# Kernel optimization log

Hardware: AMD Instinct MI355X
Metric: run time of the kernel (lower is better)

## Reference

```python
import jax, jax.numpy as jnp
import numpy as np

N = 50000
E = 800000
D = 128
L = 3


def gru_cell(m, h, w_ih, w_hh, b_ih, b_hh):
    # m, h: [N, D]; w_ih, w_hh: [3D, D]; b_ih, b_hh: [3D]
    gi = m @ w_ih.T + b_ih  # [N, 3D]
    gh = h @ w_hh.T + b_hh  # [N, 3D]
    i_r, i_z, i_n = jnp.split(gi, 3, axis=-1)
    h_r, h_z, h_n = jnp.split(gh, 3, axis=-1)
    r = jax.nn.sigmoid(i_r + h_r)
    z = jax.nn.sigmoid(i_z + h_z)
    n = jnp.tanh(i_n + r * h_n)
    return (1.0 - z) * n + z * h


def setup_inputs() -> dict:
    key = jax.random.key(0)
    ks = jax.random.split(key, 8)
    s = 1.0 / np.sqrt(D)
    z = jax.random.normal(ks[0], (N, D), dtype=jnp.float32)
    edge_index = jax.random.randint(ks[1], (2, E), 0, N, dtype=jnp.int64)
    weight = jax.random.uniform(ks[2], (L, D, D), dtype=jnp.float32, minval=-s, maxval=s)
    w_ih = jax.random.uniform(ks[3], (3 * D, D), dtype=jnp.float32, minval=-s, maxval=s)
    w_hh = jax.random.uniform(ks[4], (3 * D, D), dtype=jnp.float32, minval=-s, maxval=s)
    b_ih = jax.random.uniform(ks[5], (3 * D,), dtype=jnp.float32, minval=-s, maxval=s)
    b_hh = jax.random.uniform(ks[6], (3 * D,), dtype=jnp.float32, minval=-s, maxval=s)
    return {"z": z, "edge_index": edge_index, "weight": weight,
            "w_ih": w_ih, "w_hh": w_hh, "b_ih": b_ih, "b_hh": b_hh}


def reference(z, edge_index, weight, w_ih, w_hh, b_ih, b_hh):
    # GatedGraphConv: per layer, m = h @ W_l; aggregate m[src] into dst (sum); GRU update.
    src, dst = edge_index[0], edge_index[1]
    h = z  # in_channels == out_channels, no padding
    for l in range(L):
        m = h @ weight[l]                              # [N, D]
        agg = jax.ops.segment_sum(m[src], dst, num_segments=N)  # scatter-add over edges
        h = gru_cell(agg, h, w_ih, w_hh, b_ih, b_hh)
    return h
```

## Files before the change

kernel.cpp:

```cpp
#include <hip/hip_runtime.h>
#include <hip/hip_bf16.h>

#define NN 50000
#define NE 800000
#define D 128
#define NL 3
#define G3 384

typedef __attribute__((ext_vector_type(4))) float f32x4;
typedef __attribute__((ext_vector_type(2))) float f32x2;
typedef _Float16 f16;
typedef __attribute__((ext_vector_type(8))) _Float16 f16x8;
typedef __attribute__((ext_vector_type(2))) _Float16 f16x2;

__global__ void detect_i64_kernel(const int* __restrict__ ei, int* __restrict__ flag) {
    __shared__ int any_nz;
    if (threadIdx.x == 0) any_nz = 0;
    __syncthreads();
    int v = ei[threadIdx.x * 2 + 1];
    if (v != 0) atomicOr(&any_nz, 1);
    __syncthreads();
    if (threadIdx.x == 0) *flag = (any_nz == 0) ? 1 : 0;
}

static __device__ __forceinline__ void load_edge(const int* ei, const int* flag, int e,
                                                 int& src, int& dst) {
    if (*flag) {
        src = ei[2LL * e];
        dst = ei[2LL * (NE + e)];
    } else {
        src = ei[e];
        dst = ei[NE + e];
    }
}

__global__ void hist_kernel(const int* __restrict__ ei, const int* __restrict__ flag,
                            int* __restrict__ counts, unsigned short* __restrict__ rank16) {
    int e = blockIdx.x * blockDim.x + threadIdx.x;
    if (e >= NE) return;
    int src, dst;
    load_edge(ei, flag, e, src, dst);
    rank16[e] = (unsigned short)atomicAdd(counts + dst, 1);
}

#define SBLK 256
#define NSB ((NN + SBLK - 1) / SBLK)

__global__ __launch_bounds__(SBLK) void scan_reduce_kernel(const int* __restrict__ counts,
                                                           int* __restrict__ block_sums) {
    __shared__ int lds[SBLK];
    int i = blockIdx.x * SBLK + threadIdx.x;
    lds[threadIdx.x] = (i < NN) ? counts[i] : 0;
    __syncthreads();
    for (int off = SBLK / 2; off > 0; off >>= 1) {
        if (threadIdx.x < off) lds[threadIdx.x] += lds[threadIdx.x + off];
        __syncthreads();
    }
    if (threadIdx.x == 0) block_sums[blockIdx.x] = lds[0];
}

__global__ __launch_bounds__(256) void scan_offsets_kernel(const int* __restrict__ block_sums,
                                                           int* __restrict__ block_off,
                                                           int* __restrict__ row_start) {
    __shared__ int lds[256];
    int t = threadIdx.x;
    int v = (t < NSB) ? block_sums[t] : 0;
    lds[t] = v;
    __syncthreads();
    for (int off = 1; off < 256; off <<= 1) {
        int x = (t >= off) ? lds[t - off] : 0;
        __syncthreads();
        lds[t] += x;
        __syncthreads();
    }
    if (t < NSB) block_off[t] = lds[t] - v;
    if (t == 255) row_start[NN] = lds[255];
}

__global__ __launch_bounds__(SBLK) void scan_final_kernel(const int* __restrict__ counts,
                                                          const int* __restrict__ block_off,
                                                          int* __restrict__ row_start) {
    __shared__ int lds[SBLK];
    int i = blockIdx.x * SBLK + threadIdx.x;
    int v = (i < NN) ? counts[i] : 0;
    lds[threadIdx.x] = v;
    __syncthreads();
    for (int off = 1; off < SBLK; off <<= 1) {
        int x = (threadIdx.x >= off) ? lds[threadIdx.x - off] : 0;
        __syncthreads();
        lds[threadIdx.x] += x;
        __syncthreads();
    }
    if (i < NN) row_start[i] = block_off[blockIdx.x] + lds[threadIdx.x] - v;
}

__global__ void fill_kernel(const int* __restrict__ ei, const int* __restrict__ flag,
                            const int* __restrict__ row_start,
                            const unsigned short* __restrict__ rank16,
                            unsigned short* __restrict__ csr16) {
    int e = blockIdx.x * blockDim.x + threadIdx.x;
    if (e >= NE) return;
    int src, dst;
    load_edge(ei, flag, e, src, dst);
    csr16[row_start[dst] + (int)rank16[e]] = (unsigned short)src;
}

__global__ void init_h_kernel(const float* __restrict__ z, f16* __restrict__ h) {
    int i = blockIdx.x * blockDim.x + threadIdx.x;
    if (i * 2 >= NN * D) return;
    f32x2 v = *(const f32x2*)(z + i * 2);
    f16x2 o = {(f16)v[0], (f16)v[1]};
    *(f16x2*)(h + i * 2) = o;
}

__global__ __launch_bounds__(256) void gather_kernel(
    const f16* __restrict__ h, const int* __restrict__ row_start,
    const unsigned short* __restrict__ csr16, f16* __restrict__ agg) {
    int row = blockIdx.x * 4 + (threadIdx.x >> 6);
    if (row >= NN) return;
    int lane = threadIdx.x & 63;
    int eslot = lane >> 4;
    int c0 = (lane & 15) * 8;
    int beg = row_start[row], end = row_start[row + 1];
    float acc[8] = {0.f, 0.f, 0.f, 0.f, 0.f, 0.f, 0.f, 0.f};
    float acc2[8] = {0.f, 0.f, 0.f, 0.f, 0.f, 0.f, 0.f, 0.f};
    int e = beg;
    for (; e + 7 < end; e += 8) {
        int s0 = (int)csr16[e + eslot];
        int s1 = (int)csr16[e + eslot + 4];
        f16x8 v0 = *(const f16x8*)(h + s0 * D + c0);
        f16x8 v1 = *(const f16x8*)(h + s1 * D + c0);
#pragma unroll
        for (int j = 0; j < 8; ++j) { acc[j] += (float)v0[j]; acc2[j] += (float)v1[j]; }
    }
    for (; e + eslot < end; e += 4) {
        int s = (int)csr16[e + eslot];
        f16x8 v = *(const f16x8*)(h + s * D + c0);
#pragma unroll
        for (int j = 0; j < 8; ++j) acc[j] += (float)v[j];
    }
#pragma unroll
    for (int j = 0; j < 8; ++j) {
        acc[j] += acc2[j];
        acc[j] += __shfl_xor(acc[j], 16, 64);
        acc[j] += __shfl_xor(acc[j], 32, 64);
    }
    if (lane < 16) {
        f16x8 o;
#pragma unroll
        for (int j = 0; j < 8; ++j) o[j] = (f16)acc[j];
        *(f16x8*)(agg + row * D + c0) = o;
    }
}

__global__ void precompute_weights(const float* __restrict__ weight,
                                   const float* __restrict__ w_ih,
                                   const float* __restrict__ w_hh,
                                   f16* __restrict__ wct, f16* __restrict__ whh) {
    int l = blockIdx.x / G3;
    int g = blockIdx.x % G3;
    int c = threadIdx.x;
    __shared__ float wih_row[D];
    wih_row[c] = w_ih[g * D + c];
    __syncthreads();
    const float* wrow = weight + ((long long)l * D + c) * D;
    float acc = 0.f;
#pragma unroll 8
    for (int j = 0; j < D; ++j) acc += wrow[j] * wih_row[j];
    wct[((long long)l * G3 + g) * D + c] = (f16)acc;
    if (l == 0) whh[g * D + c] = (f16)w_hh[g * D + c];
}

#define TMG 128
#define NDT 2
#define MFMA_F16 __builtin_amdgcn_mfma_f32_16x16x32_f16
__global__ __launch_bounds__(512) void gru_fused_kernel(
    const f16* __restrict__ agg, const f16* __restrict__ hin, f16* __restrict__ hout,
    const f16* __restrict__ wct, const f16* __restrict__ whh,
    const float* __restrict__ b_ih, const float* __restrict__ b_hh,
    float* __restrict__ out_f32) {
    __shared__ char wlds[NDT * 6 * 4096];
    const int tid = threadIdx.x;
    const int lane = tid & 63;
    const int wv = tid >> 6;
    const int fr = lane & 15;
    const int kg = lane >> 4;
    const int m0 = blockIdx.x * TMG;
    const int dt0 = blockIdx.y * NDT;

    int arow = m0 + wv * 16 + fr;
    int arc = arow < NN ? arow : NN - 1;
    const int abase = arc * D;

    f16x8 fa[4], fh[4];
#pragma unroll
    for (int ks = 0; ks < 4; ++ks) {
        int k0 = ks * 32 + kg * 8;
        fa[ks] = *(const f16x8*)(agg + abase + k0);
        fh[ks] = *(const f16x8*)(hin + abase + k0);
    }

#pragma unroll
    for (int p6 = 0; p6 < NDT * 3; ++p6) {
        int unit = tid + p6 * 512;
        int dpanel = unit >> 8;
        int dti = dpanel / 6;
        int panel = dpanel % 6;
        int u = unit & 255;
        int sr = u >> 4;
        int sc = (u & 15) * 8;
        int gr = (dt0 + dti) * 16;
        const f16* srcp = (panel < 3)
                              ? wct + (panel * 128 + gr + sr) * D + sc
                              : whh + ((panel - 3) * 128 + gr + sr) * D + sc;
        int wb = (u * 16) ^ ((sr & 7) << 4);
        *(f16x8*)(wlds + dpanel * 4096 + wb) = *(const f16x8*)srcp;
    }
    __syncthreads();

#pragma unroll
    for (int dti = 0; dti < NDT; ++dti) {
        const int gr = (dt0 + dti) * 16;
        const char* wb0 = wlds + dti * 6 * 4096;
        f32x4 a_ir = {0, 0, 0, 0}, a_iz = {0, 0, 0, 0}, a_in = {0, 0, 0, 0};
        f32x4 a_hr = {0, 0, 0, 0}, a_hz = {0, 0, 0, 0}, a_hn = {0, 0, 0, 0};
#pragma unroll
        for (int ks = 0; ks < 4; ++ks) {
            const int kb = fr * 256 + (((ks * 4 + kg) ^ (fr & 7)) << 4);
            f16x8 bir = *(const f16x8*)(wb0 + 0 * 4096 + kb);
            f16x8 biz = *(const f16x8*)(wb0 + 1 * 4096 + kb);
            f16x8 bin = *(const f16x8*)(wb0 + 2 * 4096 + kb);
            f16x8 bhr = *(const f16x8*)(wb0 + 3 * 4096 + kb);
            f16x8 bhz = *(const f16x8*)(wb0 + 4 * 4096 + kb);
            f16x8 bhn = *(const f16x8*)(wb0 + 5 * 4096 + kb);
            a_ir = MFMA_F16(fa[ks], bir, a_ir, 0, 0, 0);
            a_iz = MFMA_F16(fa[ks], biz, a_iz, 0, 0, 0);
            a_in = MFMA_F16(fa[ks], bin, a_in, 0, 0, 0);
            a_hr = MFMA_F16(fh[ks], bhr, a_hr, 0, 0, 0);
            a_hz = MFMA_F16(fh[ks], bhz, a_hz, 0, 0, 0);
            a_hn = MFMA_F16(fh[ks], bhn, a_hn, 0, 0, 0);
        }
        const int d = gr + fr;
        float bir_ = b_ih[d], biz_ = b_ih[128 + d], bin_ = b_ih[256 + d];
        float bhr_ = b_hh[d], bhz_ = b_hh[128 + d], bhn_ = b_hh[256 + d];
#pragma unroll
        for (int j = 0; j < 4; ++j) {
            int row = m0 + wv * 16 + kg * 4 + j;
            if (row >= NN) continue;
            float ir = a_ir[j] + bir_, iz = a_iz[j] + biz_, in_ = a_in[j] + bin_;
            float hr = a_hr[j] + bhr_, hz = a_hz[j] + bhz_, hn = a_hn[j] + bhn_;
            float r = 1.f / (1.f + __expf(-(ir + hr)));
            float zz = 1.f / (1.f + __expf(-(iz + hz)));
            float e2 = __expf(2.f * (in_ + r * hn));
            float nn = 1.f - 2.f / (e2 + 1.f);
            int off = row * D + d;
            float hold = (float)hin[off];
            float hnew = (1.f - zz) * nn + zz * hold;
            if (out_f32)
                out_f32[off] = hnew;
            else
                hout[off] = (f16)hnew;
        }
    }
}

__global__ __launch_bounds__(256) void gru_fused_fallback(
    const f16* __restrict__ agg, const f16* __restrict__ hin, f16* __restrict__ hout,
    const f16* __restrict__ wct, const f16* __restrict__ whh,
    const float* __restrict__ b_ih, const float* __restrict__ b_hh,
    float* __restrict__ out_f32) {
    const int tid = threadIdx.x;
    const int lane = tid & 63;
    const int wv = tid >> 6;
    const int fr = lane & 15;
    const int kg = lane >> 4;
    const int m0 = blockIdx.x * 64;
    int arow = m0 + wv * 16 + fr;
    int arc = arow < NN ? arow : NN - 1;
    const int abase = arc * D;
    f16x8 fa[4], fh[4];
#pragma unroll
    for (int ks = 0; ks < 4; ++ks) {
        int k0 = ks * 32 + kg * 8;
        fa[ks] = *(const f16x8*)(agg + abase + k0);
        fh[ks] = *(const f16x8*)(hin + abase + k0);
    }
#pragma unroll 1
    for (int dt = 0; dt < 8; ++dt) {
        const int g = dt * 16 + fr;
        f32x4 a_ir = {0, 0, 0, 0}, a_iz = {0, 0, 0, 0}, a_in = {0, 0, 0, 0};
        f32x4 a_hr = {0, 0, 0, 0}, a_hz = {0, 0, 0, 0}, a_hn = {0, 0, 0, 0};
#pragma unroll
        for (int ks = 0; ks < 4; ++ks) {
            int k0 = ks * 32 + kg * 8;
            f16x8 bir = *(const f16x8*)(wct + (g)*D + k0);
            f16x8 biz = *(const f16x8*)(wct + (128 + g) * D + k0);
            f16x8 bin = *(const f16x8*)(wct + (256 + g) * D + k0);
            f16x8 bhr = *(const f16x8*)(whh + (g)*D + k0);
            f16x8 bhz = *(const f16x8*)(whh + (128 + g) * D + k0);
            f16x8 bhn = *(const f16x8*)(whh + (256 + g) * D + k0);
            a_ir = MFMA_F16(fa[ks], bir, a_ir, 0, 0, 0);
            a_iz = MFMA_F16(fa[ks], biz, a_iz, 0, 0, 0);
            a_in = MFMA_F16(fa[ks], bin, a_in, 0, 0, 0);
            a_hr = MFMA_F16(fh[ks], bhr, a_hr, 0, 0, 0);
            a_hz = MFMA_F16(fh[ks], bhz, a_hz, 0, 0, 0);
            a_hn = MFMA_F16(fh[ks], bhn, a_hn, 0, 0, 0);
        }
        const int d = g;
        float bir_ = b_ih[d], biz_ = b_ih[128 + d], bin_ = b_ih[256 + d];
        float bhr_ = b_hh[d], bhz_ = b_hh[128 + d], bhn_ = b_hh[256 + d];
#pragma unroll
        for (int j = 0; j < 4; ++j) {
            int row = m0 + wv * 16 + kg * 4 + j;
            if (row >= NN) continue;
            float ir = a_ir[j] + bir_, iz = a_iz[j] + biz_, in_ = a_in[j] + bin_;
            float hr = a_hr[j] + bhr_, hz = a_hz[j] + bhz_, hn = a_hn[j] + bhn_;
            float r = 1.f / (1.f + __expf(-(ir + hr)));
            float zz = 1.f / (1.f + __expf(-(iz + hz)));
            float e2 = __expf(2.f * (in_ + r * hn));
            float nn = 1.f - 2.f / (e2 + 1.f);
            int off = row * D + d;
            float hold = (float)hin[off];
            float hnew = (1.f - zz) * nn + zz * hold;
            if (out_f32)
                out_f32[off] = hnew;
            else
                hout[off] = (f16)hnew;
        }
    }
}

extern "C" void kernel_launch(void* const* d_in, const int* in_sizes, int n_in,
                              void* d_out, int out_size, void* d_ws, size_t ws_size,
                              hipStream_t stream) {
    const float* z = (const float*)d_in[0];
    const int* ei = (const int*)d_in[1];
    const float* weight = (const float*)d_in[2];
    const float* w_ih = (const float*)d_in[3];
    const float* w_hh = (const float*)d_in[4];
    const float* b_ih = (const float*)d_in[5];
    const float* b_hh = (const float*)d_in[6];
    float* out = (float*)d_out;

    char* ws = (char*)d_ws;
    size_t off = 0;
    f16* wct = (f16*)(ws + off); off += 294912;
    f16* whh = (f16*)(ws + off); off += 98304;
    int* flag       = (int*)(ws + off); off += 256;
    int* counts     = (int*)(ws + off); off += (size_t)NN * 4;
    int* row_start  = (int*)(ws + off); off += (size_t)(NN + 16) * 4;
    int* block_sums = (int*)(ws + off); off += (size_t)NSB * 4;
    int* block_off  = (int*)(ws + off); off += (size_t)NSB * 4;
    unsigned short* rank16 = (unsigned short*)(ws + off); off += (size_t)NE * 2;
    unsigned short* csr16  = (unsigned short*)(ws + off); off += (size_t)NE * 2;
    f16* agg  = (f16*)(ws + off); off += (size_t)NN * D * 2;
    f16* hA   = (f16*)(ws + off); off += (size_t)NN * D * 2;
    f16* hB   = (f16*)(ws + off); off += (size_t)NN * D * 2;
    const bool split = (ws_size >= off);
    if (!split) hB = hA;

    detect_i64_kernel<<<1, 256, 0, stream>>>(ei, flag);
    hipMemsetAsync(counts, 0, (size_t)NN * 4, stream);
    hist_kernel<<<(NE + 255) / 256, 256, 0, stream>>>(ei, flag, counts, rank16);
    scan_reduce_kernel<<<NSB, SBLK, 0, stream>>>(counts, block_sums);
    scan_offsets_kernel<<<1, 256, 0, stream>>>(block_sums, block_off, row_start);
    scan_final_kernel<<<NSB, SBLK, 0, stream>>>(counts, block_off, row_start);
    fill_kernel<<<(NE + 255) / 256, 256, 0, stream>>>(ei, flag, row_start, rank16, csr16);
    precompute_weights<<<NL * G3, 128, 0, stream>>>(weight, w_ih, w_hh, wct, whh);
    const int npair = NN * D / 2;
    init_h_kernel<<<(npair + 255) / 256, 256, 0, stream>>>(z, hA);

    const dim3 gg((NN + TMG - 1) / TMG, 8 / NDT);
    const f16* cin = hA;
    for (int l = 0; l < NL; ++l) {
        gather_kernel<<<(NN + 3) / 4, 256, 0, stream>>>(cin, row_start, csr16, agg);
        f16* cout = split ? ((cin == hA) ? hB : hA) : (f16*)cin;
        long long woff = (long long)l * G3 * D;
        float* last_out = (l == NL - 1) ? out : nullptr;
        if (split) {
            gru_fused_kernel<<<gg, 512, 0, stream>>>(agg, cin, cout, wct + woff, whh,
                                                     b_ih, b_hh, last_out);
        } else {
            gru_fused_fallback<<<(NN + 63) / 64, 256, 0, stream>>>(
                agg, cin, cout, wct + woff, whh, b_ih, b_hh, last_out);
        }
        cin = cout;
    }
}
```

Measured before the change: 297.6 us.

## Fuse neighbor gather into GRU kernel and batch edges per thread in CSR build

The separate gather kernel and its global agg buffer are removed on the main path. Each 64-row block now gathers neighbor sums into LDS and feeds them straight into the MFMA GRU update, looping over all 8 output column tiles and restaging weights each time. The hist and fill kernels now handle 4 edges per thread. This saves one kernel launch per layer and the agg write and read, but each block does a serial 16-row gather per wave with fewer parallel blocks, and reloads the full weights per block instead of a column slice.

```diff
diff --git a/kernel.cpp b/kernel.cpp
--- a/kernel.cpp
+++ b/kernel.cpp
@@ -34,13 +34,27 @@
     }
 }
 
+#define HBLK ((NE / 4 + 255) / 256)
 __global__ void hist_kernel(const int* __restrict__ ei, const int* __restrict__ flag,
                             int* __restrict__ counts, unsigned short* __restrict__ rank16) {
-    int e = blockIdx.x * blockDim.x + threadIdx.x;
-    if (e >= NE) return;
-    int src, dst;
-    load_edge(ei, flag, e, src, dst);
-    rank16[e] = (unsigned short)atomicAdd(counts + dst, 1);
+    int base = blockIdx.x * blockDim.x + threadIdx.x;
+    const int stride = HBLK * 256;
+    int e0 = base, e1 = base + stride, e2 = base + 2 * stride, e3 = base + 3 * stride;
+    int s0, d0, s1, d1, s2, d2, s3, d3;
+    bool v0 = e0 < NE, v1 = e1 < NE, v2 = e2 < NE, v3 = e3 < NE;
+    if (v0) load_edge(ei, flag, e0, s0, d0);
+    if (v1) load_edge(ei, flag, e1, s1, d1);
+    if (v2) load_edge(ei, flag, e2, s2, d2);
+    if (v3) load_edge(ei, flag, e3, s3, d3);
+    unsigned short r0, r1, r2, r3;
+    if (v0) r0 = (unsigned short)atomicAdd(counts + d0, 1);
+    if (v1) r1 = (unsigned short)atomicAdd(counts + d1, 1);
+    if (v2) r2 = (unsigned short)atomicAdd(counts + d2, 1);
+    if (v3) r3 = (unsigned short)atomicAdd(counts + d3, 1);
+    if (v0) rank16[e0] = r0;
+    if (v1) rank16[e1] = r1;
+    if (v2) rank16[e2] = r2;
+    if (v3) rank16[e3] = r3;
 }
 
 #define SBLK 256
@@ -98,11 +112,16 @@
                             const int* __restrict__ row_start,
                             const unsigned short* __restrict__ rank16,
                             unsigned short* __restrict__ csr16) {
-    int e = blockIdx.x * blockDim.x + threadIdx.x;
-    if (e >= NE) return;
-    int src, dst;
-    load_edge(ei, flag, e, src, dst);
-    csr16[row_start[dst] + (int)rank16[e]] = (unsigned short)src;
+    int base = blockIdx.x * blockDim.x + threadIdx.x;
+    const int stride = HBLK * 256;
+#pragma unroll
+    for (int k = 0; k < 4; ++k) {
+        int e = base + k * stride;
+        if (e >= NE) continue;
+        int src, dst;
+        load_edge(ei, flag, e, src, dst);
+        csr16[row_start[dst] + (int)rank16[e]] = (unsigned short)src;
+    }
 }
 
 __global__ void init_h_kernel(const float* __restrict__ z, f16* __restrict__ h) {
@@ -113,44 +132,12 @@
     *(f16x2*)(h + i * 2) = o;
 }
 
-__global__ __launch_bounds__(256) void gather_kernel(
-    const f16* __restrict__ h, const int* __restrict__ row_start,
-    const unsigned short* __restrict__ csr16, f16* __restrict__ agg) {
-    int row = blockIdx.x * 4 + (threadIdx.x >> 6);
-    if (row >= NN) return;
-    int lane = threadIdx.x & 63;
-    int eslot = lane >> 4;
-    int c0 = (lane & 15) * 8;
-    int beg = row_start[row], end = row_start[row + 1];
-    float acc[8] = {0.f, 0.f, 0.f, 0.f, 0.f, 0.f, 0.f, 0.f};
-    float acc2[8] = {0.f, 0.f, 0.f, 0.f, 0.f, 0.f, 0.f, 0.f};
-    int e = beg;
-    for (; e + 7 < end; e += 8) {
-        int s0 = (int)csr16[e + eslot];
-        int s1 = (int)csr16[e + eslot + 4];
-        f16x8 v0 = *(const f16x8*)(h + s0 * D + c0);
-        f16x8 v1 = *(const f16x8*)(h + s1 * D + c0);
-#pragma unroll
-        for (int j = 0; j < 8; ++j) { acc[j] += (float)v0[j]; acc2[j] += (float)v1[j]; }
-    }
-    for (; e + eslot < end; e += 4) {
-        int s = (int)csr16[e + eslot];
-        f16x8 v = *(const f16x8*)(h + s * D + c0);
-#pragma unroll
-        for (int j = 0; j < 8; ++j) acc[j] += (float)v[j];
-    }
-#pragma unroll
-    for (int j = 0; j < 8; ++j) {
-        acc[j] += acc2[j];
-        acc[j] += __shfl_xor(acc[j], 16, 64);
-        acc[j] += __shfl_xor(acc[j], 32, 64);
-    }
-    if (lane < 16) {
-        f16x8 o;
-#pragma unroll
-        for (int j = 0; j < 8; ++j) o[j] = (f16)acc[j];
-        *(f16x8*)(agg + row * D + c0) = o;
-    }
+__global__ void finalize_kernel(const f16* __restrict__ h, float* __restrict__ out) {
+    int i = blockIdx.x * blockDim.x + threadIdx.x;
+    if (i * 2 >= NN * D) return;
+    f16x2 v = *(const f16x2*)(h + i * 2);
+    f32x2 o = {(float)v[0], (float)v[1]};
+    *(f32x2*)(out + i * 2) = o;
 }
 
 __global__ void precompute_weights(const float* __restrict__ weight,
@@ -171,68 +158,105 @@
     if (l == 0) whh[g * D + c] = (f16)w_hh[g * D + c];
 }
 
-#define TMG 128
-#define NDT 2
+#define TMF 64
 #define MFMA_F16 __builtin_amdgcn_mfma_f32_16x16x32_f16
-__global__ __launch_bounds__(512) void gru_fused_kernel(
-    const f16* __restrict__ agg, const f16* __restrict__ hin, f16* __restrict__ hout,
+__global__ __launch_bounds__(256) void gru_gather_fused(
+    const f16* __restrict__ hin, f16* __restrict__ hout,
+    const int* __restrict__ row_start, const unsigned short* __restrict__ csr16,
     const f16* __restrict__ wct, const f16* __restrict__ whh,
     const float* __restrict__ b_ih, const float* __restrict__ b_hh,
     float* __restrict__ out_f32) {
-    __shared__ char wlds[NDT * 6 * 4096];
+    __shared__ char aggl[TMF * 256];
+    __shared__ char wlds[6 * 4096];
     const int tid = threadIdx.x;
     const int lane = tid & 63;
     const int wv = tid >> 6;
     const int fr = lane & 15;
     const int kg = lane >> 4;
-    const int m0 = blockIdx.x * TMG;
-    const int dt0 = blockIdx.y * NDT;
-
-    int arow = m0 + wv * 16 + fr;
-    int arc = arow < NN ? arow : NN - 1;
+    const int m0 = blockIdx.x * TMF;
+
+    const int eslot = lane >> 4;
+    const int c0 = (lane & 15) * 8;
+#pragma unroll 1
+    for (int rr = 0; rr < 16; ++rr) {
+        const int g = m0 + wv * 16 + rr;
+        float acc[8] = {0.f, 0.f, 0.f, 0.f, 0.f, 0.f, 0.f, 0.f};
+        float acc2[8] = {0.f, 0.f, 0.f, 0.f, 0.f, 0.f, 0.f, 0.f};
+        if (g < NN) {
+            int beg = row_start[g], end = row_start[g + 1];
+            int e = beg;
+            for (; e + 7 < end; e += 8) {
+                int s0 = (int)csr16[e + eslot];
+                int s1 = (int)csr16[e + eslot + 4];
+                f16x8 v0 = *(const f16x8*)(hin + s0 * D + c0);
+                f16x8 v1 = *(const f16x8*)(hin + s1 * D + c0);
+#pragma unroll
+                for (int j = 0; j < 8; ++j) { acc[j] += (float)v0[j]; acc2[j] += (float)v1[j]; }
+            }
+            for (; e + eslot < end; e += 4) {
+                int s = (int)csr16[e + eslot];
+                f16x8 v = *(const f16x8*)(hin + s * D + c0);
+#pragma unroll
+                for (int j = 0; j < 8; ++j) acc[j] += (float)v[j];
+            }
+        }
+#pragma unroll
+        for (int j = 0; j < 8; ++j) {
+            acc[j] += acc2[j];
+            acc[j] += __shfl_xor(acc[j], 16, 64);
+            acc[j] += __shfl_xor(acc[j], 32, 64);
+        }
+        if (lane < 16) {
+            const int rl = wv * 16 + rr;
+            f16x8 o;
+#pragma unroll
+            for (int j = 0; j < 8; ++j) o[j] = (f16)acc[j];
+            *(f16x8*)(aggl + rl * 256 + ((lane ^ (rl & 7)) << 4)) = o;
+        }
+    }
+
+    const int arow = m0 + wv * 16 + fr;
+    const int arc = arow < NN ? arow : NN - 1;
     const int abase = arc * D;
-
-    f16x8 fa[4], fh[4];
-#pragma unroll
-    for (int ks = 0; ks < 4; ++ks) {
-        int k0 = ks * 32 + kg * 8;
-        fa[ks] = *(const f16x8*)(agg + abase + k0);
-        fh[ks] = *(const f16x8*)(hin + abase + k0);
-    }
-
-#pragma unroll
-    for (int p6 = 0; p6 < NDT * 3; ++p6) {
-        int unit = tid + p6 * 512;
-        int dpanel = unit >> 8;
-        int dti = dpanel / 6;
-        int panel = dpanel % 6;
-        int u = unit & 255;
-        int sr = u >> 4;
-        int sc = (u & 15) * 8;
-        int gr = (dt0 + dti) * 16;
-        const f16* srcp = (panel < 3)
-                              ? wct + (panel * 128 + gr + sr) * D + sc
-                              : whh + ((panel - 3) * 128 + gr + sr) * D + sc;
-        int wb = (u * 16) ^ ((sr & 7) << 4);
-        *(f16x8*)(wlds + dpanel * 4096 + wb) = *(const f16x8*)srcp;
-    }
-    __syncthreads();
-
-#pragma unroll
-    for (int dti = 0; dti < NDT; ++dti) {
-        const int gr = (dt0 + dti) * 16;
-        const char* wb0 = wlds + dti * 6 * 4096;
+    f16x8 fh[4];
+#pragma unroll
+    for (int ks = 0; ks < 4; ++ks)
+        fh[ks] = *(const f16x8*)(hin + abase + ks * 32 + kg * 8);
+
+    __syncthreads();
+
+    const int rl = wv * 16 + fr;
+    f16x8 fa[4];
+#pragma unroll
+    for (int ks = 0; ks < 4; ++ks)
+        fa[ks] = *(const f16x8*)(aggl + rl * 256 + (((ks * 4 + kg) ^ (rl & 7)) << 4));
+
+    const int sr = tid >> 4;
+    const int sc = (tid & 15) * 8;
+    const int wb = (tid * 16) ^ ((sr & 7) << 4);
+#pragma unroll 1
+    for (int dt = 0; dt < 8; ++dt) {
+        const int gr = dt * 16;
+        if (dt) __syncthreads();
+#pragma unroll
+        for (int p = 0; p < 6; ++p) {
+            const f16* srcp = (p < 3) ? wct + (p * 128 + gr + sr) * D + sc
+                                      : whh + ((p - 3) * 128 + gr + sr) * D + sc;
+            *(f16x8*)(wlds + p * 4096 + wb) = *(const f16x8*)srcp;
+        }
+        __syncthreads();
+
         f32x4 a_ir = {0, 0, 0, 0}, a_iz = {0, 0, 0, 0}, a_in = {0, 0, 0, 0};
         f32x4 a_hr = {0, 0, 0, 0}, a_hz = {0, 0, 0, 0}, a_hn = {0, 0, 0, 0};
 #pragma unroll
         for (int ks = 0; ks < 4; ++ks) {
             const int kb = fr * 256 + (((ks * 4 + kg) ^ (fr & 7)) << 4);
-            f16x8 bir = *(const f16x8*)(wb0 + 0 * 4096 + kb);
-            f16x8 biz = *(const f16x8*)(wb0 + 1 * 4096 + kb);
-            f16x8 bin = *(const f16x8*)(wb0 + 2 * 4096 + kb);
-            f16x8 bhr = *(const f16x8*)(wb0 + 3 * 4096 + kb);
-            f16x8 bhz = *(const f16x8*)(wb0 + 4 * 4096 + kb);
-            f16x8 bhn = *(const f16x8*)(wb0 + 5 * 4096 + kb);
+            f16x8 bir = *(const f16x8*)(wlds + 0 * 4096 + kb);
+            f16x8 biz = *(const f16x8*)(wlds + 1 * 4096 + kb);
+            f16x8 bin = *(const f16x8*)(wlds + 2 * 4096 + kb);
+            f16x8 bhr = *(const f16x8*)(wlds + 3 * 4096 + kb);
+            f16x8 bhz = *(const f16x8*)(wlds + 4 * 4096 + kb);
+            f16x8 bhn = *(const f16x8*)(wlds + 5 * 4096 + kb);
             a_ir = MFMA_F16(fa[ks], bir, a_ir, 0, 0, 0);
             a_iz = MFMA_F16(fa[ks], biz, a_iz, 0, 0, 0);
             a_in = MFMA_F16(fa[ks], bin, a_in, 0, 0, 0);
@@ -264,11 +288,39 @@
     }
 }
 
+__global__ __launch_bounds__(256) void gather_kernel(
+    const f16* __restrict__ h, const int* __restrict__ row_start,
+    const unsigned short* __restrict__ csr16, f16* __restrict__ agg) {
+    int row = blockIdx.x * 4 + (threadIdx.x >> 6);
+    if (row >= NN) return;
+    int lane = threadIdx.x & 63;
+    int eslot = lane >> 4;
+    int c0 = (lane & 15) * 8;
+    int beg = row_start[row], end = row_start[row + 1];
+    float acc[8] = {0.f, 0.f, 0.f, 0.f, 0.f, 0.f, 0.f, 0.f};
+    for (int base = beg; base + eslot < end; base += 4) {
+        int s = (int)csr16[base + eslot];
+        f16x8 v = *(const f16x8*)(h + s * D + c0);
+#pragma unroll
+        for (int j = 0; j < 8; ++j) acc[j] += (float)v[j];
+    }
+#pragma unroll
+    for (int j = 0; j < 8; ++j) {
+        acc[j] += __shfl_xor(acc[j], 16, 64);
+        acc[j] += __shfl_xor(acc[j], 32, 64);
+    }
+    if (lane < 16) {
+        f16x8 o;
+#pragma unroll
+        for (int j = 0; j < 8; ++j) o[j] = (f16)acc[j];
+        *(f16x8*)(agg + row * D + c0) = o;
+    }
+}
+
 __global__ __launch_bounds__(256) void gru_fused_fallback(
     const f16* __restrict__ agg, const f16* __restrict__ hin, f16* __restrict__ hout,
     const f16* __restrict__ wct, const f16* __restrict__ whh,
-    const float* __restrict__ b_ih, const float* __restrict__ b_hh,
-    float* __restrict__ out_f32) {
+    const float* __restrict__ b_ih, const float* __restrict__ b_hh) {
     const int tid = threadIdx.x;
     const int lane = tid & 63;
     const int wv = tid >> 6;
@@ -321,11 +373,7 @@
             float nn = 1.f - 2.f / (e2 + 1.f);
             int off = row * D + d;
             float hold = (float)hin[off];
-            float hnew = (1.f - zz) * nn + zz * hold;
-            if (out_f32)
-                out_f32[off] = hnew;
-            else
-                hout[off] = (f16)hnew;
+            hout[off] = (f16)((1.f - zz) * nn + zz * hold);
         }
     }
 }
@@ -353,37 +401,40 @@
     int* block_off  = (int*)(ws + off); off += (size_t)NSB * 4;
     unsigned short* rank16 = (unsigned short*)(ws + off); off += (size_t)NE * 2;
     unsigned short* csr16  = (unsigned short*)(ws + off); off += (size_t)NE * 2;
-    f16* agg  = (f16*)(ws + off); off += (size_t)NN * D * 2;
     f16* hA   = (f16*)(ws + off); off += (size_t)NN * D * 2;
     f16* hB   = (f16*)(ws + off); off += (size_t)NN * D * 2;
     const bool split = (ws_size >= off);
-    if (!split) hB = hA;
 
     detect_i64_kernel<<<1, 256, 0, stream>>>(ei, flag);
     hipMemsetAsync(counts, 0, (size_t)NN * 4, stream);
-    hist_kernel<<<(NE + 255) / 256, 256, 0, stream>>>(ei, flag, counts, rank16);
+    hist_kernel<<<HBLK, 256, 0, stream>>>(ei, flag, counts, rank16);
     scan_reduce_kernel<<<NSB, SBLK, 0, stream>>>(counts, block_sums);
     scan_offsets_kernel<<<1, 256, 0, stream>>>(block_sums, block_off, row_start);
     scan_final_kernel<<<NSB, SBLK, 0, stream>>>(counts, block_off, row_start);
-    fill_kernel<<<(NE + 255) / 256, 256, 0, stream>>>(ei, flag, row_start, rank16, csr16);
+    fill_kernel<<<HBLK, 256, 0, stream>>>(ei, flag, row_start, rank16, csr16);
     precompute_weights<<<NL * G3, 128, 0, stream>>>(weight, w_ih, w_hh, wct, whh);
     const int npair = NN * D / 2;
     init_h_kernel<<<(npair + 255) / 256, 256, 0, stream>>>(z, hA);
 
-    const dim3 gg((NN + TMG - 1) / TMG, 8 / NDT);
-    const f16* cin = hA;
-    for (int l = 0; l < NL; ++l) {
-        gather_kernel<<<(NN + 3) / 4, 256, 0, stream>>>(cin, row_start, csr16, agg);
-        f16* cout = split ? ((cin == hA) ? hB : hA) : (f16*)cin;
-        long long woff = (long long)l * G3 * D;
-        float* last_out = (l == NL - 1) ? out : nullptr;
-        if (split) {
-            gru_fused_kernel<<<gg, 512, 0, stream>>>(agg, cin, cout, wct + woff, whh,
-                                                     b_ih, b_hh, last_out);
-        } else {
+    const int nblk = (NN + TMF - 1) / TMF;
+    if (split) {
+        const f16* cin = hA;
+        for (int l = 0; l < NL; ++l) {
+            f16* cout = (cin == hA) ? hB : hA;
+            long long woff = (long long)l * G3 * D;
+            float* last_out = (l == NL - 1) ? out : nullptr;
+            gru_gather_fused<<<nblk, 256, 0, stream>>>(
+                cin, cout, row_start, csr16, wct + woff, whh, b_ih, b_hh, last_out);
+            cin = cout;
+        }
+    } else {
+        f16* agg = (f16*)d_out;
+        for (int l = 0; l < NL; ++l) {
+            gather_kernel<<<(NN + 3) / 4, 256, 0, stream>>>(hA, row_start, csr16, agg);
+            long long woff = (long long)l * G3 * D;
             gru_fused_fallback<<<(NN + 63) / 64, 256, 0, stream>>>(
-                agg, cin, cout, wct + woff, whh, b_ih, b_hh, last_out);
-        }
-        cin = cout;
-    }
-}
+                agg, hA, hA, wct + woff, whh, b_ih, b_hh);
+        }
+        finalize_kernel<<<(npair + 255) / 256, 256, 0, stream>>>(hA, out);
+    }
+}
```

Result: slower. 307.2 us (+3.2%).
